# Optimization experiments

Measured on AMD Instinct MI355X. Metric: run time of the kernel, lower is better.

## Reference

```python
import jax, jax.numpy as jnp
import numpy as np

IN_DIM = 256
LN_EPS = 1e-05


def _xavier(key, shape):
    fan_in, fan_out = shape[1], shape[0]
    a = np.sqrt(6.0 / (fan_in + fan_out)).astype(np.float32)
    return jax.random.uniform(key, shape, jnp.float32, -a, a)


def setup_inputs() -> dict:
    key = jax.random.key(0)
    ks = jax.random.split(key, 4)
    B, C, H, W = 32, IN_DIM, 32, 32
    x = jax.random.normal(ks[0], (B, C, H, W), jnp.float32)
    y = jax.random.normal(ks[1], (B, C, H, W), jnp.float32)
    # nn.MultiheadAttention in_proj: rows [0:C] -> Wq, [C:2C] -> Wk (V/out_proj
    # never influence the returned attention weights, so omitted).
    Wq = _xavier(ks[2], (C, C))
    Wk = _xavier(ks[3], (C, C))
    bq = jnp.zeros((C,), jnp.float32)
    bk = jnp.zeros((C,), jnp.float32)
    # norm1 LayerNorm affine params (norm2 is unused in forward).
    gamma = jnp.ones((C,), jnp.float32)
    beta = jnp.zeros((C,), jnp.float32)
    return {"x": x, "y": y, "gamma": gamma, "beta": beta,
            "Wq": Wq, "Wk": Wk, "bq": bq, "bk": bk}


def _layernorm(t, gamma, beta):
    mu = jnp.mean(t, axis=-1, keepdims=True)
    var = jnp.mean(jnp.square(t - mu), axis=-1, keepdims=True)
    return (t - mu) * jax.lax.rsqrt(var + LN_EPS) * gamma + beta


def reference(x, y, gamma, beta, Wq, Wk, bq, bk):
    B, C = x.shape[0], x.shape[1]
    # [B,C,H,W] -> [B, N, C]
    xs = x.reshape(B, C, -1).transpose(0, 2, 1)
    ys = y.reshape(B, C, -1).transpose(0, 2, 1)
    q = _layernorm(xs, gamma, beta) @ Wq.T + bq   # [B,N,C]
    k = _layernorm(ys, gamma, beta) @ Wk.T + bk   # [B,N,C]
    scale = 1.0 / np.sqrt(C).astype(np.float32)   # single head: head_dim = C
    scores = jnp.einsum('bnc,bmc->bnm', q, k) * scale  # [B,N,N]
    w = jax.nn.softmax(scores, axis=-1)
    # module returns weight.diagonal(dim1=1, dim2=2) -> [B, N]
    return jnp.diagonal(w, axis1=1, axis2=2)
```

## Files before the change

kernel.cpp:

```cpp
#include <hip/hip_runtime.h>
#include <math.h>

#define BATCH 32
#define CDIM  256
#define NDIM  1024
#define BN    (BATCH * NDIM)
#define BNC   ((size_t)BATCH * NDIM * CDIM)
#define LN_EPSF 1e-5f
#define SCALE 0.0625f

typedef __attribute__((ext_vector_type(8))) __bf16 bf16x8;
typedef __attribute__((ext_vector_type(4))) float f32x4;
typedef __attribute__((ext_vector_type(4))) unsigned short ushort4v;

static __device__ __forceinline__ unsigned short f2bf(float f) {
  unsigned u = __float_as_uint(f);
  unsigned r = (u + 0x7FFFu + ((u >> 16) & 1u)) >> 16;
  return (unsigned short)r;
}
static __device__ __forceinline__ float bf2f(unsigned short h) {
  return __uint_as_float(((unsigned)h) << 16);
}
static __device__ __forceinline__ void gload16(const void* g, void* l) {
  __builtin_amdgcn_global_load_lds((const __attribute__((address_space(1))) void*)g,
                                   (__attribute__((address_space(3))) void*)l, 16, 0, 0);
}


__global__ __launch_bounds__(256) void wsplit_k(const float* __restrict__ Wq,
                                                const float* __restrict__ Wk,
                                                unsigned short* __restrict__ wp) {
  int idx = blockIdx.x * 256 + threadIdx.x;
  float vq = Wq[idx];
  unsigned short hq = f2bf(vq);
  wp[idx] = hq;
  wp[65536 + idx] = f2bf(vq - bf2f(hq));
  float vk = Wk[idx];
  unsigned short hk = f2bf(vk);
  wp[131072 + idx] = hk;
  wp[196608 + idx] = f2bf(vk - bf2f(hk));
}

__global__ __launch_bounds__(256) void proj_k(const float* __restrict__ x,
                                              const float* __restrict__ y,
                                              const float* __restrict__ gamma,
                                              const float* __restrict__ beta,
                                              const float* __restrict__ bq,
                                              const float* __restrict__ bk,
                                              const unsigned short* __restrict__ wp,
                                              unsigned short* __restrict__ planes) {
  __shared__ unsigned short Lh[64][264];
  __shared__ unsigned short Ll[64][264];
  __shared__ float psum[16][64], psq[16][64];
  __shared__ float mu[64], ri[64], gl[CDIM], bl[CDIM], bias_s[CDIM];

  const int t = threadIdx.x;
  const int bz = blockIdx.y;
  const int b = bz >> 1, which = bz & 1;
  const int n0 = blockIdx.x * 64;
  const float* src = which ? y : x;

  gl[t] = gamma[t];
  bl[t] = beta[t];
  bias_s[t] = (which ? bk : bq)[t];

  const int nq = (t & 15) * 4;
  const int cs = (t >> 4) * 16;
  float4 xr[16];
#pragma unroll
  for (int i = 0; i < 16; ++i)
    xr[i] = *(const float4*)(src + ((size_t)b * CDIM + cs + i) * NDIM + n0 + nq);

  {
    float s[4] = {0.f, 0.f, 0.f, 0.f}, q[4] = {0.f, 0.f, 0.f, 0.f};
#pragma unroll
    for (int i = 0; i < 16; ++i) {
      float v0 = xr[i].x, v1 = xr[i].y, v2 = xr[i].z, v3 = xr[i].w;
      s[0] += v0; q[0] += v0 * v0;
      s[1] += v1; q[1] += v1 * v1;
      s[2] += v2; q[2] += v2 * v2;
      s[3] += v3; q[3] += v3 * v3;
    }
#pragma unroll
    for (int j = 0; j < 4; ++j) {
      psum[t >> 4][nq + j] = s[j];
      psq[t >> 4][nq + j] = q[j];
    }
  }
  __syncthreads();
  if (t < 64) {
    float S = 0.f, Q = 0.f;
#pragma unroll
    for (int s16 = 0; s16 < 16; ++s16) { S += psum[s16][t]; Q += psq[s16][t]; }
    float m = S * (1.f / CDIM);
    mu[t] = m;
    ri[t] = rsqrtf(fmaxf(Q * (1.f / CDIM) - m * m, 0.f) + LN_EPSF);
  }
  __syncthreads();

  {
    float mj[4], rj[4];
#pragma unroll
    for (int j = 0; j < 4; ++j) { mj[j] = mu[nq + j]; rj[j] = ri[nq + j]; }
#pragma unroll
    for (int k = 0; k < 8; ++k) {
      const int c0 = cs + 2 * k, c1 = c0 + 1;
      const float g0 = gl[c0], b0 = bl[c0], g1 = gl[c1], b1 = bl[c1];
      const float u0[4] = {xr[2 * k].x, xr[2 * k].y, xr[2 * k].z, xr[2 * k].w};
      const float u1[4] = {xr[2 * k + 1].x, xr[2 * k + 1].y, xr[2 * k + 1].z, xr[2 * k + 1].w};
#pragma unroll
      for (int j = 0; j < 4; ++j) {
        float v0 = (u0[j] - mj[j]) * rj[j] * g0 + b0;
        float v1 = (u1[j] - mj[j]) * rj[j] * g1 + b1;
        unsigned short h0 = f2bf(v0), h1 = f2bf(v1);
        unsigned short e0 = f2bf(v0 - bf2f(h0)), e1 = f2bf(v1 - bf2f(h1));
        *(unsigned*)&Lh[nq + j][c0] = ((unsigned)h1 << 16) | h0;
        *(unsigned*)&Ll[nq + j][c0] = ((unsigned)e1 << 16) | e0;
      }
    }
  }
  __syncthreads();

  const int w = t >> 6, l = t & 63;
  const int l15 = l & 15, l4 = l >> 4;
  const int co_base = w * 64;
  const unsigned short* Wh = wp + (size_t)which * 131072;
  const unsigned short* Wl = Wh + 65536;

  f32x4 acc[4][4];
#pragma unroll
  for (int i = 0; i < 4; ++i)
#pragma unroll
    for (int j = 0; j < 4; ++j) acc[i][j] = (f32x4){0.f, 0.f, 0.f, 0.f};

#pragma unroll
  for (int kt = 0; kt < 8; ++kt) {
    const int c0 = kt * 32;
    bf16x8 Ah[4], Al[4], Bh[4], Bl[4];
#pragma unroll
    for (int i = 0; i < 4; ++i) {
      size_t off = (size_t)(co_base + i * 16 + l15) * CDIM + c0 + l4 * 8;
      Ah[i] = *(const bf16x8*)(Wh + off);
      Al[i] = *(const bf16x8*)(Wl + off);
    }
#pragma unroll
    for (int j = 0; j < 4; ++j) {
      Bh[j] = *(const bf16x8*)&Lh[j * 16 + l15][c0 + l4 * 8];
      Bl[j] = *(const bf16x8*)&Ll[j * 16 + l15][c0 + l4 * 8];
    }
#pragma unroll
    for (int i = 0; i < 4; ++i)
#pragma unroll
      for (int j = 0; j < 4; ++j) {
        acc[i][j] = __builtin_amdgcn_mfma_f32_16x16x32_bf16(Ah[i], Bh[j], acc[i][j], 0, 0, 0);
        acc[i][j] = __builtin_amdgcn_mfma_f32_16x16x32_bf16(Ah[i], Bl[j], acc[i][j], 0, 0, 0);
        acc[i][j] = __builtin_amdgcn_mfma_f32_16x16x32_bf16(Al[i], Bh[j], acc[i][j], 0, 0, 0);
      }
  }

  unsigned short* ph = planes + (size_t)which * (2 * BNC);
  unsigned short* pl = ph + BNC;
#pragma unroll
  for (int i = 0; i < 4; ++i) {
    const int co4 = co_base + i * 16 + l4 * 4;
    float bias4[4];
#pragma unroll
    for (int r = 0; r < 4; ++r) bias4[r] = bias_s[co4 + r];
#pragma unroll
    for (int j = 0; j < 4; ++j) {
      size_t base = ((size_t)b * NDIM + n0 + j * 16 + l15) * CDIM + co4;
      ushort4v hs, ls;
#pragma unroll
      for (int r = 0; r < 4; ++r) {
        float v = acc[i][j][r] + bias4[r];
        unsigned short h = f2bf(v);
        hs[r] = h;
        ls[r] = f2bf(v - bf2f(h));
      }
      *(ushort4v*)(ph + base) = hs;
      *(ushort4v*)(pl + base) = ls;
    }
  }
}

__global__ __launch_bounds__(128, 2) void attn_k(const unsigned short* __restrict__ planes,
                                                 float* __restrict__ outp) {
  const unsigned short* qh = planes;
  const unsigned short* ql = planes + BNC;
  __shared__ unsigned short kbuf[2][8192];

  const int p = blockIdx.x;
  const int b = (p & 7) * 4 + ((p >> 3) & 3);
  const int n0 = (p >> 5) * 64;
  const int t = threadIdx.x;
  const int w = t >> 6;
  const int l = t & 63;
  const int l15 = l & 15, l4 = l >> 4;

  bf16x8 ah[2][8], al[2][8];
#pragma unroll
  for (int rf = 0; rf < 2; ++rf) {
    size_t rowbase = ((size_t)b * NDIM + n0 + w * 32 + rf * 16 + l15) * CDIM + l4 * 8;
#pragma unroll
    for (int kq = 0; kq < 8; ++kq) {
      ah[rf][kq] = *(const bf16x8*)(qh + rowbase + kq * 32);
      al[rf][kq] = *(const bf16x8*)(ql + rowbase + kq * 32);
    }
  }

  const unsigned short* kb = planes + 2 * BNC + (size_t)b * NDIM * CDIM;
  const unsigned short* lb = planes + 3 * BNC + (size_t)b * NDIM * CDIM;

  auto stage = [&](int buf, int tt) {
    const int mt = tt >> 2, kc = tt & 3;
#pragma unroll
    for (int ii = 0; ii < 8; ++ii) {
      const int chunk = w * 8 + ii;
      const int cf = chunk & 3, kf = (chunk >> 2) & 1, pl = chunk >> 3;
      size_t g = (size_t)(mt * 64 + cf * 16 + l15) * CDIM + kc * 64 + kf * 32 + l4 * 8;
      gload16((pl ? lb : kb) + g, &kbuf[buf][chunk * 512]);
    }
  };

  float M[8], S[8], dval[8];
#pragma unroll
  for (int i = 0; i < 8; ++i) { M[i] = -1e30f; S[i] = 0.f; dval[i] = 0.f; }

  stage(0, 0);
  __syncthreads();
  int cur = 0;

  for (int mt = 0; mt < 16; ++mt) {
    f32x4 acc[2][4];
#pragma unroll
    for (int rf = 0; rf < 2; ++rf)
#pragma unroll
      for (int cf = 0; cf < 4; ++cf) acc[rf][cf] = (f32x4){0.f, 0.f, 0.f, 0.f};

    for (int kc = 0; kc < 4; ++kc) {
      const int tt = mt * 4 + kc;
      if (tt + 1 < 64) stage(cur ^ 1, tt + 1);
#pragma unroll
      for (int kf = 0; kf < 2; ++kf) {
        const int kq = kc * 2 + kf;
#pragma unroll
        for (int cf = 0; cf < 4; ++cf) {
          bf16x8 Bh = *(const bf16x8*)&kbuf[cur][(kf * 4 + cf) * 512 + l * 8];
          bf16x8 Bl = *(const bf16x8*)&kbuf[cur][((2 + kf) * 4 + cf) * 512 + l * 8];
#pragma unroll
          for (int rf = 0; rf < 2; ++rf) {
            acc[rf][cf] = __builtin_amdgcn_mfma_f32_16x16x32_bf16(ah[rf][kq], Bh, acc[rf][cf], 0, 0, 0);
            acc[rf][cf] = __builtin_amdgcn_mfma_f32_16x16x32_bf16(ah[rf][kq], Bl, acc[rf][cf], 0, 0, 0);
            acc[rf][cf] = __builtin_amdgcn_mfma_f32_16x16x32_bf16(al[rf][kq], Bh, acc[rf][cf], 0, 0, 0);
          }
        }
      }
      __syncthreads();
      cur ^= 1;
    }

#pragma unroll
    for (int rf = 0; rf < 2; ++rf) {
#pragma unroll
      for (int r = 0; r < 4; ++r) {
        const int idx = rf * 4 + r;
        const int n = n0 + w * 32 + rf * 16 + l4 * 4 + r;
        float tm = -1e30f;
#pragma unroll
        for (int cf = 0; cf < 4; ++cf) tm = fmaxf(tm, acc[rf][cf][r]);
        tm *= SCALE;
#pragma unroll
        for (int off = 8; off >= 1; off >>= 1) tm = fmaxf(tm, __shfl_xor(tm, off));
        const float Mn = fmaxf(M[idx], tm);
        float ps = 0.f;
#pragma unroll
        for (int cf = 0; cf < 4; ++cf) ps += __expf(acc[rf][cf][r] * SCALE - Mn);
#pragma unroll
        for (int off = 8; off >= 1; off >>= 1) ps += __shfl_xor(ps, off);
        S[idx] = S[idx] * __expf(M[idx] - Mn) + ps;
        M[idx] = Mn;
#pragma unroll
        for (int cf = 0; cf < 4; ++cf)
          if (mt * 64 + cf * 16 + l15 == n) dval[idx] = acc[rf][cf][r] * SCALE;
      }
    }
  }

#pragma unroll
  for (int rf = 0; rf < 2; ++rf)
#pragma unroll
    for (int r = 0; r < 4; ++r) {
      const int idx = rf * 4 + r;
      const int n = n0 + w * 32 + rf * 16 + l4 * 4 + r;
      if (l15 == l4 * 4 + r)
        outp[(size_t)b * NDIM + n] = __expf(dval[idx] - M[idx]) / S[idx];
    }
}

extern "C" void kernel_launch(void* const* d_in, const int* in_sizes, int n_in,
                              void* d_out, int out_size, void* d_ws, size_t ws_size,
                              hipStream_t stream) {
  (void)in_sizes; (void)n_in; (void)out_size; (void)ws_size;
  const float* x     = (const float*)d_in[0];
  const float* y     = (const float*)d_in[1];
  const float* gamma = (const float*)d_in[2];
  const float* beta  = (const float*)d_in[3];
  const float* Wq    = (const float*)d_in[4];
  const float* Wk    = (const float*)d_in[5];
  const float* bq    = (const float*)d_in[6];
  const float* bk    = (const float*)d_in[7];
  float* out = (float*)d_out;

  unsigned short* wp = (unsigned short*)d_ws;
  unsigned short* planes = wp + 262144;

  wsplit_k<<<256, 256, 0, stream>>>(Wq, Wk, wp);

  dim3 g2(NDIM / 64, BATCH * 2);
  proj_k<<<g2, 256, 0, stream>>>(x, y, gamma, beta, bq, bk, wp, planes);

  attn_k<<<512, 128, 0, stream>>>(planes, out);
}
```

Measured before the change: 250.4 us.

## Split attention keys across two blocks and merge softmax partials

Each attention block now covers 128 query rows with 256 threads (4 waves), and the key dimension is split in two halves across blocks. Each block writes per-row running max, sum and the diagonal score to workspace, and a new merge kernel combines the two halves into the final softmax diagonal. The aim is to reuse each staged K tile across more query rows and keep the grid parallel while shortening each block's key loop. The cost is an extra kernel launch and a round trip of partial results through global memory.

```diff
diff --git a/kernel.cpp b/kernel.cpp
--- a/kernel.cpp
+++ b/kernel.cpp
@@ -183,15 +183,19 @@
   }
 }
 
-__global__ __launch_bounds__(128, 2) void attn_k(const unsigned short* __restrict__ planes,
-                                                 float* __restrict__ outp) {
+__global__ __launch_bounds__(256, 2) void attn_k(const unsigned short* __restrict__ planes,
+                                                 float* __restrict__ part) {
   const unsigned short* qh = planes;
   const unsigned short* ql = planes + BNC;
   __shared__ unsigned short kbuf[2][8192];
 
   const int p = blockIdx.x;
   const int b = (p & 7) * 4 + ((p >> 3) & 3);
-  const int n0 = (p >> 5) * 64;
+  const int rest = p >> 5;
+  const int qt = rest & 7;
+  const int ks = rest >> 3;
+  const int n0 = qt * 128;
+  const int k0 = ks * 512;
   const int t = threadIdx.x;
   const int w = t >> 6;
   const int l = t & 63;
@@ -214,10 +218,10 @@
   auto stage = [&](int buf, int tt) {
     const int mt = tt >> 2, kc = tt & 3;
 #pragma unroll
-    for (int ii = 0; ii < 8; ++ii) {
-      const int chunk = w * 8 + ii;
-      const int cf = chunk & 3, kf = (chunk >> 2) & 1, pl = chunk >> 3;
-      size_t g = (size_t)(mt * 64 + cf * 16 + l15) * CDIM + kc * 64 + kf * 32 + l4 * 8;
+    for (int ii = 0; ii < 4; ++ii) {
+      const int chunk = w * 4 + ii;
+      const int f = chunk & 3, kf = (chunk >> 2) & 1, pl = chunk >> 3;
+      size_t g = (size_t)(k0 + mt * 64 + f * 16 + l15) * CDIM + kc * 64 + kf * 32 + l4 * 8;
       gload16((pl ? lb : kb) + g, &kbuf[buf][chunk * 512]);
     }
   };
@@ -230,7 +234,7 @@
   __syncthreads();
   int cur = 0;
 
-  for (int mt = 0; mt < 16; ++mt) {
+  for (int mt = 0; mt < 8; ++mt) {
     f32x4 acc[2][4];
 #pragma unroll
     for (int rf = 0; rf < 2; ++rf)
@@ -239,14 +243,14 @@
 
     for (int kc = 0; kc < 4; ++kc) {
       const int tt = mt * 4 + kc;
-      if (tt + 1 < 64) stage(cur ^ 1, tt + 1);
+      if (tt + 1 < 32) stage(cur ^ 1, tt + 1);
 #pragma unroll
       for (int kf = 0; kf < 2; ++kf) {
         const int kq = kc * 2 + kf;
 #pragma unroll
         for (int cf = 0; cf < 4; ++cf) {
           bf16x8 Bh = *(const bf16x8*)&kbuf[cur][(kf * 4 + cf) * 512 + l * 8];
-          bf16x8 Bl = *(const bf16x8*)&kbuf[cur][((2 + kf) * 4 + cf) * 512 + l * 8];
+          bf16x8 Bl = *(const bf16x8*)&kbuf[cur][(8 + kf * 4 + cf) * 512 + l * 8];
 #pragma unroll
           for (int rf = 0; rf < 2; ++rf) {
             acc[rf][cf] = __builtin_amdgcn_mfma_f32_16x16x32_bf16(ah[rf][kq], Bh, acc[rf][cf], 0, 0, 0);
@@ -281,20 +285,37 @@
         M[idx] = Mn;
 #pragma unroll
         for (int cf = 0; cf < 4; ++cf)
-          if (mt * 64 + cf * 16 + l15 == n) dval[idx] = acc[rf][cf][r] * SCALE;
-      }
-    }
-  }
-
+          if (k0 + mt * 64 + cf * 16 + l15 == n) dval[idx] = acc[rf][cf][r] * SCALE;
+      }
+    }
+  }
+
+  float* Mp = part;
+  float* Sp = part + 2 * BN;
+  float* dv = part + 4 * BN;
 #pragma unroll
   for (int rf = 0; rf < 2; ++rf)
 #pragma unroll
     for (int r = 0; r < 4; ++r) {
       const int idx = rf * 4 + r;
       const int n = n0 + w * 32 + rf * 16 + l4 * 4 + r;
-      if (l15 == l4 * 4 + r)
-        outp[(size_t)b * NDIM + n] = __expf(dval[idx] - M[idx]) / S[idx];
-    }
+      if (l15 == l4 * 4 + r) {
+        Mp[ks * BN + b * NDIM + n] = M[idx];
+        Sp[ks * BN + b * NDIM + n] = S[idx];
+        if ((n >> 9) == ks) dv[b * NDIM + n] = dval[idx];
+      }
+    }
+}
+
+__global__ __launch_bounds__(256) void merge_k(const float* __restrict__ part,
+                                               float* __restrict__ outp) {
+  const int gid = blockIdx.x * 256 + threadIdx.x;
+  const float M0 = part[gid], M1 = part[BN + gid];
+  const float S0 = part[2 * BN + gid], S1 = part[3 * BN + gid];
+  const float d = part[4 * BN + gid];
+  const float Mf = fmaxf(M0, M1);
+  const float Sf = S0 * __expf(M0 - Mf) + S1 * __expf(M1 - Mf);
+  outp[gid] = __expf(d - Mf) / Sf;
 }
 
 extern "C" void kernel_launch(void* const* d_in, const int* in_sizes, int n_in,
@@ -313,11 +334,14 @@
 
   unsigned short* wp = (unsigned short*)d_ws;
   unsigned short* planes = wp + 262144;
+  float* part = (float*)(planes + 4 * BNC);
 
   wsplit_k<<<256, 256, 0, stream>>>(Wq, Wk, wp);
 
   dim3 g2(NDIM / 64, BATCH * 2);
   proj_k<<<g2, 256, 0, stream>>>(x, y, gamma, beta, bq, bk, wp, planes);
 
-  attn_k<<<512, 128, 0, stream>>>(planes, out);
-}
+  attn_k<<<512, 256, 0, stream>>>(planes, part);
+
+  merge_k<<<BN / 256, 256, 0, stream>>>(part, out);
+}
```

Result: faster. 215.3 us (-14.0%).
